# Kernel tuning notes

Hardware: AMD Instinct MI355X
Metric: run time of the kernel (lower is better)

The kernel has to match this reference:

```python
import jax, jax.numpy as jnp
import numpy as np

H = 8   # hidden size
I = 4   # input size
O = 4   # output size


def setup_inputs() -> dict:
    key = jax.random.key(0)
    ks = jax.random.split(key, 7)
    B, T = 4096, 2048
    s_ih = 1.0 / np.sqrt(H)
    x = jax.random.normal(ks[0], (B, T, I), dtype=jnp.float32)
    W_ih = jax.random.uniform(ks[1], (3 * H, I), minval=-s_ih, maxval=s_ih, dtype=jnp.float32)
    W_hh = jax.random.uniform(ks[2], (3 * H, H), minval=-s_ih, maxval=s_ih, dtype=jnp.float32)
    b_ih = jax.random.uniform(ks[3], (3 * H,), minval=-s_ih, maxval=s_ih, dtype=jnp.float32)
    b_hh = jax.random.uniform(ks[4], (3 * H,), minval=-s_ih, maxval=s_ih, dtype=jnp.float32)
    W_fc = jax.random.uniform(ks[5], (O, H), minval=-s_ih, maxval=s_ih, dtype=jnp.float32)
    b_fc = jax.random.uniform(ks[6], (O,), minval=-s_ih, maxval=s_ih, dtype=jnp.float32)
    return {"x": x, "W_ih": W_ih, "W_hh": W_hh, "b_ih": b_ih, "b_hh": b_hh,
            "W_fc": W_fc, "b_fc": b_fc}


def _gru(x, W_ih, W_hh, b_ih, b_hh):
    # x: [B, T, I] (batch_first). Precompute input-gate projections once.
    xg = jnp.einsum('bti,gi->btg', x, W_ih) + b_ih          # [B, T, 3H]
    B = x.shape[0]
    h0 = jnp.zeros((B, H), dtype=x.dtype)

    def step(h, xg_t):
        gh = h @ W_hh.T + b_hh                               # [B, 3H]
        xr, xz, xn = xg_t[:, :H], xg_t[:, H:2 * H], xg_t[:, 2 * H:]
        hr, hz, hn = gh[:, :H], gh[:, H:2 * H], gh[:, 2 * H:]
        r = jax.nn.sigmoid(xr + hr)
        z = jax.nn.sigmoid(xz + hz)
        n = jnp.tanh(xn + r * hn)
        h_new = (1.0 - z) * n + z * h
        return h_new, h_new

    _, hs = jax.lax.scan(step, h0, jnp.swapaxes(xg, 0, 1))  # hs: [T, B, H]
    return jnp.swapaxes(hs, 0, 1)                            # [B, T, H]


def reference(x, W_ih, W_hh, b_ih, b_hh, W_fc, b_fc):
    gru_out = _gru(x, W_ih, W_hh, b_ih, b_hh)                # [B, T, H]
    return jnp.einsum('bth,oh->bto', gru_out, W_fc) + b_fc   # [B, T, O]
```

## Files before the change

### kernel.cpp

```cpp
#include <hip/hip_runtime.h>


#define GRU_T 2048
#define GRU_H 8
#define GRU_I 4
#define GRU_O 4
#define PFD   8

#define DPP_ROR(n) (0x120 + (n))

template <int CTRL>
__device__ __forceinline__ float dpp_movf(float v) {
    return __int_as_float(
        __builtin_amdgcn_mov_dpp(__float_as_int(v), CTRL, 0xf, 0xf, true));
}

__device__ __forceinline__ float fast_rcp(float x)  { return __builtin_amdgcn_rcpf(x); }
__device__ __forceinline__ float fast_exp2(float x) { return __builtin_amdgcn_exp2f(x); }

__global__ __launch_bounds__(64, 1) void gru_fc_kernel(
    const float* __restrict__ x,
    const float* __restrict__ W_ih,
    const float* __restrict__ W_hh,
    const float* __restrict__ b_ih,
    const float* __restrict__ b_hh,
    const float* __restrict__ W_fc,
    const float* __restrict__ b_fc,
    float* __restrict__ out)
{
    const int tid = blockIdx.x * 64 + (int)threadIdx.x;
    const int b   = tid >> 4;
    const int q   = tid & 15;
    const int g   = (q >> 3) & 1;
    const int m   = q & 7;
    const int o   = q & 3;
    const bool hi = (q & 8) != 0;

    const float SR = -1.4426950408889634f;
    const float SZ =  1.4426950408889634f;
    const float SN =  2.8853900817779268f;

    const float SG   = g ? SZ : SR;
    const int   gate = g ? 1 : 0;

    float whA[8], whn[8], wf[8];
#pragma unroll
    for (int r = 0; r < 8; ++r) {
        const int k = (m - r) & 7;
        whA[r] = SG * W_hh[(gate * GRU_H + m) * GRU_H + k];
        whn[r] = SN * W_hh[(2 * GRU_H + m) * GRU_H + k];
        wf[r]  = W_fc[o * GRU_H + k];
    }
    float wiA[4], win[4];
#pragma unroll
    for (int k = 0; k < 4; ++k) {
        wiA[k] = SG * W_ih[(gate * GRU_H + m) * GRU_I + k];
        win[k] = SN * W_ih[(2 * GRU_H + m) * GRU_I + k];
    }
    const float bA  = SG * (b_ih[gate * GRU_H + m] + b_hh[gate * GRU_H + m]);
    const float bxn = SN * b_ih[2 * GRU_H + m];
    const float bhn = SN * b_hh[2 * GRU_H + m];
    const float bo  = b_fc[o];

    float hprev = 0.0f;
    float bank0 = 0.0f, bank1 = 0.0f, bank2 = 0.0f;

    const float4* __restrict__ xp = reinterpret_cast<const float4*>(x) + (size_t)b * GRU_T;
    float* __restrict__ op = out + (size_t)b * GRU_T * GRU_O + q;

    float4 bufA[PFD], bufB[PFD];
#pragma unroll
    for (int j = 0; j < PFD; ++j) bufA[j] = xp[j];

#define GRU_STEP(XC, TCUR, JM)                                                 \
    do {                                                                       \
        const float4 xc = (XC);                                                \
               \
        const float xA  = fmaf(wiA[1], xc.y, fmaf(wiA[0], xc.x, bA));          \
        const float xB  = fmaf(wiA[3], xc.w, wiA[2] * xc.z);                   \
        const float xn_ = fmaf(win[3], xc.w, fmaf(win[2], xc.z,                \
                          fmaf(win[1], xc.y, fmaf(win[0], xc.x, bxn))));       \
        const float onemh = 1.0f - hprev;                                      \
                            \
        const float r1 = dpp_movf<DPP_ROR(1)>(hprev);                          \
        const float r2 = dpp_movf<DPP_ROR(2)>(hprev);                          \
        const float r3 = dpp_movf<DPP_ROR(3)>(hprev);                          \
        const float r4 = dpp_movf<DPP_ROR(4)>(hprev);                          \
        const float r5 = dpp_movf<DPP_ROR(5)>(hprev);                          \
        const float r6 = dpp_movf<DPP_ROR(6)>(hprev);                          \
        const float r7 = dpp_movf<DPP_ROR(7)>(hprev);                          \
                        \
        const float tA = fmaf(whA[1], r1, fmaf(whA[0], hprev, xA));            \
        const float tB = fmaf(whA[3], r3, fmaf(whA[2], r2, xB));               \
        const float tC = fmaf(whA[5], r5, whA[4] * r4);                        \
        const float tD = fmaf(whA[7], r7, whA[6] * r6);                        \
        const float aOwn = (tA + tB) + (tC + tD);                              \
                           \
        const float sOwn = fast_rcp(1.0f + fast_exp2(aOwn));                   \
                        \
        const float sSib = dpp_movf<DPP_ROR(8)>(sOwn);                         \
        const float rg   = hi ? sSib : sOwn;                                   \
        const float omz  = hi ? sOwn : sSib;                                   \
                         \
        const float nA = fmaf(whn[3], r3, fmaf(whn[2], r2,                     \
                         fmaf(whn[1], r1, fmaf(whn[0], hprev, bhn))));         \
        const float nB = fmaf(whn[7], r7, fmaf(whn[6], r6,                     \
                         fmaf(whn[5], r5, whn[4] * r4)));                      \
        const float ahn = nA + nB;                                             \
                         \
        const float fA = fmaf(wf[3], r3, fmaf(wf[2], r2,                       \
                         fmaf(wf[1], r1, fmaf(wf[0], hprev, bo))));            \
        const float fB = fmaf(wf[7], r7, fmaf(wf[6], r6,                       \
                         fmaf(wf[5], r5, wf[4] * r4)));                        \
        const float fc = fA + fB;                                              \
                                              \
        const float c1  = fmaf(omz, onemh, hprev);                             \
        const float m2z = -2.0f * omz;                                         \
        const float yn  = fmaf(rg, ahn, xn_);                                  \
        const float u   = fast_rcp(1.0f + fast_exp2(yn));                      \
        hprev = fmaf(m2z, u, c1);                 \
                   \
        if (((JM) & 3) == 1)      bank0 = fc;                                  \
        else if (((JM) & 3) == 2) bank1 = fc;                                  \
        else if (((JM) & 3) == 3) bank2 = fc;                                  \
        else if ((TCUR) != 0) {                                                \
            const float v01 = (q & 4) ? bank1 : bank0;                         \
            const float v23 = (q & 4) ? fc    : bank2;                         \
            const float val = (q & 8) ? v23   : v01;                           \
            op[(size_t)((TCUR) - 4) * GRU_O] = val;                            \
        }                                                                      \
    } while (0)

    for (int tb = 0; tb < GRU_T; tb += 2 * PFD) {
#pragma unroll
        for (int j = 0; j < PFD; ++j) bufB[j] = xp[tb + PFD + j];
#pragma unroll
        for (int j = 0; j < PFD; ++j) GRU_STEP(bufA[j], tb + j, j);
        const int tn = (tb + 2 * PFD) & (GRU_T - 1);
#pragma unroll
        for (int j = 0; j < PFD; ++j) bufA[j] = xp[tn + j];
#pragma unroll
        for (int j = 0; j < PFD; ++j) GRU_STEP(bufB[j], tb + PFD + j, j);
    }

    {
        const float r1 = dpp_movf<DPP_ROR(1)>(hprev);
        const float r2 = dpp_movf<DPP_ROR(2)>(hprev);
        const float r3 = dpp_movf<DPP_ROR(3)>(hprev);
        const float r4 = dpp_movf<DPP_ROR(4)>(hprev);
        const float r5 = dpp_movf<DPP_ROR(5)>(hprev);
        const float r6 = dpp_movf<DPP_ROR(6)>(hprev);
        const float r7 = dpp_movf<DPP_ROR(7)>(hprev);
        const float fA = fmaf(wf[3], r3, fmaf(wf[2], r2,
                         fmaf(wf[1], r1, fmaf(wf[0], hprev, bo))));
        const float fB = fmaf(wf[7], r7, fmaf(wf[6], r6,
                         fmaf(wf[5], r5, wf[4] * r4)));
        const float fc = fA + fB;
        const float v01 = (q & 4) ? bank1 : bank0;
        const float v23 = (q & 4) ? fc    : bank2;
        const float val = (q & 8) ? v23   : v01;
        op[(size_t)(GRU_T - 4) * GRU_O] = val;
    }
#undef GRU_STEP
}

extern "C" void kernel_launch(void* const* d_in, const int* in_sizes, int n_in,
                              void* d_out, int out_size, void* d_ws, size_t ws_size,
                              hipStream_t stream) {
    const float* x    = (const float*)d_in[0];
    const float* W_ih = (const float*)d_in[1];
    const float* W_hh = (const float*)d_in[2];
    const float* b_ih = (const float*)d_in[3];
    const float* b_hh = (const float*)d_in[4];
    const float* W_fc = (const float*)d_in[5];
    const float* b_fc = (const float*)d_in[6];
    float* out = (float*)d_out;

    const int B = in_sizes[0] / (GRU_T * GRU_I);
    dim3 grid((unsigned)(B * 16 / 64)), block(64);
    hipLaunchKernelGGL(gru_fc_kernel, grid, block, 0, stream,
                       x, W_ih, W_hh, b_ih, b_hh, W_fc, b_fc, out);
}
```

Before: 422.9 us.

## Interleave two batch recurrences per thread and halve the grid

Each 16-lane group now runs the GRU recurrence for two batch elements, interleaving their steps so the two independent dependency chains can hide each other's DPP and transcendental latency. The grid shrinks by half and the prefetch depth drops from 8 to 4 per stream to keep register use in check. The cost is that fewer wavefronts are launched, so some SIMDs may sit idle. Each wave also does twice the serial work.

```diff
diff --git a/kernel.cpp b/kernel.cpp
--- a/kernel.cpp
+++ b/kernel.cpp
@@ -5,7 +5,7 @@
 #define GRU_H 8
 #define GRU_I 4
 #define GRU_O 4
-#define PFD   8
+#define PFD   4
 
 #define DPP_ROR(n) (0x120 + (n))
 
@@ -29,12 +29,15 @@
     float* __restrict__ out)
 {
     const int tid = blockIdx.x * 64 + (int)threadIdx.x;
-    const int b   = tid >> 4;
+    const int G   = tid >> 4;
     const int q   = tid & 15;
     const int g   = (q >> 3) & 1;
     const int m   = q & 7;
     const int o   = q & 3;
     const bool hi = (q & 8) != 0;
+
+    const int eA = 2 * G;
+    const int eB = 2 * G + 1;
 
     const float SR = -1.4426950408889634f;
     const float SZ =  1.4426950408889634f;
@@ -62,106 +65,123 @@
     const float bhn = SN * b_hh[2 * GRU_H + m];
     const float bo  = b_fc[o];
 
-    float hprev = 0.0f;
-    float bank0 = 0.0f, bank1 = 0.0f, bank2 = 0.0f;
-
-    const float4* __restrict__ xp = reinterpret_cast<const float4*>(x) + (size_t)b * GRU_T;
-    float* __restrict__ op = out + (size_t)b * GRU_T * GRU_O + q;
-
-    float4 bufA[PFD], bufB[PFD];
-#pragma unroll
-    for (int j = 0; j < PFD; ++j) bufA[j] = xp[j];
-
-#define GRU_STEP(XC, TCUR, JM)                                                 \
+    float hprevA = 0.0f, bank0A = 0.0f, bank1A = 0.0f, bank2A = 0.0f;
+    float hprevB = 0.0f, bank0B = 0.0f, bank1B = 0.0f, bank2B = 0.0f;
+
+    const float4* __restrict__ xpA = reinterpret_cast<const float4*>(x) + (size_t)eA * GRU_T;
+    const float4* __restrict__ xpB = reinterpret_cast<const float4*>(x) + (size_t)eB * GRU_T;
+    float* __restrict__ opA = out + (size_t)eA * GRU_T * GRU_O + q;
+    float* __restrict__ opB = out + (size_t)eB * GRU_T * GRU_O + q;
+
+    float4 pingA[PFD], pongA[PFD], pingB[PFD], pongB[PFD];
+#pragma unroll
+    for (int j = 0; j < PFD; ++j) { pingA[j] = xpA[j]; pingB[j] = xpB[j]; }
+
+#define GRU_STEP(S, XC, TCUR, JM)                                              \
     do {                                                                       \
         const float4 xc = (XC);                                                \
-               \
-        const float xA  = fmaf(wiA[1], xc.y, fmaf(wiA[0], xc.x, bA));          \
-        const float xB  = fmaf(wiA[3], xc.w, wiA[2] * xc.z);                   \
-        const float xn_ = fmaf(win[3], xc.w, fmaf(win[2], xc.z,                \
-                          fmaf(win[1], xc.y, fmaf(win[0], xc.x, bxn))));       \
-        const float onemh = 1.0f - hprev;                                      \
+        const float xA_  = fmaf(wiA[1], xc.y, fmaf(wiA[0], xc.x, bA));         \
+        const float xB_  = fmaf(wiA[3], xc.w, wiA[2] * xc.z);                  \
+        const float xn_  = fmaf(win[3], xc.w, fmaf(win[2], xc.z,               \
+                           fmaf(win[1], xc.y, fmaf(win[0], xc.x, bxn))));      \
+        const float onemh = 1.0f - hprev##S;                                   \
                             \
-        const float r1 = dpp_movf<DPP_ROR(1)>(hprev);                          \
-        const float r2 = dpp_movf<DPP_ROR(2)>(hprev);                          \
-        const float r3 = dpp_movf<DPP_ROR(3)>(hprev);                          \
-        const float r4 = dpp_movf<DPP_ROR(4)>(hprev);                          \
-        const float r5 = dpp_movf<DPP_ROR(5)>(hprev);                          \
-        const float r6 = dpp_movf<DPP_ROR(6)>(hprev);                          \
-        const float r7 = dpp_movf<DPP_ROR(7)>(hprev);                          \
+        const float r1 = dpp_movf<DPP_ROR(1)>(hprev##S);                       \
+        const float r2 = dpp_movf<DPP_ROR(2)>(hprev##S);                       \
+        const float r3 = dpp_movf<DPP_ROR(3)>(hprev##S);                       \
+        const float r4 = dpp_movf<DPP_ROR(4)>(hprev##S);                       \
+        const float r5 = dpp_movf<DPP_ROR(5)>(hprev##S);                       \
+        const float r6 = dpp_movf<DPP_ROR(6)>(hprev##S);                       \
+        const float r7 = dpp_movf<DPP_ROR(7)>(hprev##S);                       \
                         \
-        const float tA = fmaf(whA[1], r1, fmaf(whA[0], hprev, xA));            \
-        const float tB = fmaf(whA[3], r3, fmaf(whA[2], r2, xB));               \
+        const float tA = fmaf(whA[1], r1, fmaf(whA[0], hprev##S, xA_));        \
+        const float tB = fmaf(whA[3], r3, fmaf(whA[2], r2, xB_));              \
         const float tC = fmaf(whA[5], r5, whA[4] * r4);                        \
         const float tD = fmaf(whA[7], r7, whA[6] * r6);                        \
         const float aOwn = (tA + tB) + (tC + tD);                              \
-                           \
+            \
         const float sOwn = fast_rcp(1.0f + fast_exp2(aOwn));                   \
-                        \
         const float sSib = dpp_movf<DPP_ROR(8)>(sOwn);                         \
         const float rg   = hi ? sSib : sOwn;                                   \
         const float omz  = hi ? sOwn : sSib;                                   \
-                         \
+                                                             \
         const float nA = fmaf(whn[3], r3, fmaf(whn[2], r2,                     \
-                         fmaf(whn[1], r1, fmaf(whn[0], hprev, bhn))));         \
+                         fmaf(whn[1], r1, fmaf(whn[0], hprev##S, bhn))));      \
         const float nB = fmaf(whn[7], r7, fmaf(whn[6], r6,                     \
                          fmaf(whn[5], r5, whn[4] * r4)));                      \
         const float ahn = nA + nB;                                             \
                          \
         const float fA = fmaf(wf[3], r3, fmaf(wf[2], r2,                       \
-                         fmaf(wf[1], r1, fmaf(wf[0], hprev, bo))));            \
+                         fmaf(wf[1], r1, fmaf(wf[0], hprev##S, bo))));         \
         const float fB = fmaf(wf[7], r7, fmaf(wf[6], r6,                       \
                          fmaf(wf[5], r5, wf[4] * r4)));                        \
-        const float fc = fA + fB;                                              \
-                                              \
-        const float c1  = fmaf(omz, onemh, hprev);                             \
+        const float fcv = fA + fB;                                             \
+                                                                     \
+        const float c1  = fmaf(omz, onemh, hprev##S);                          \
         const float m2z = -2.0f * omz;                                         \
         const float yn  = fmaf(rg, ahn, xn_);                                  \
         const float u   = fast_rcp(1.0f + fast_exp2(yn));                      \
-        hprev = fmaf(m2z, u, c1);                 \
-                   \
-        if (((JM) & 3) == 1)      bank0 = fc;                                  \
-        else if (((JM) & 3) == 2) bank1 = fc;                                  \
-        else if (((JM) & 3) == 3) bank2 = fc;                                  \
+        hprev##S = fmaf(m2z, u, c1);              \
+                         \
+        if ((JM) == 1)      bank0##S = fcv;                                    \
+        else if ((JM) == 2) bank1##S = fcv;                                    \
+        else if ((JM) == 3) bank2##S = fcv;                                    \
         else if ((TCUR) != 0) {                                                \
-            const float v01 = (q & 4) ? bank1 : bank0;                         \
-            const float v23 = (q & 4) ? fc    : bank2;                         \
-            const float val = (q & 8) ? v23   : v01;                           \
-            op[(size_t)((TCUR) - 4) * GRU_O] = val;                            \
+            const float v01 = (q & 4) ? bank1##S : bank0##S;                   \
+            const float v23 = (q & 4) ? fcv      : bank2##S;                   \
+            const float val = (q & 8) ? v23      : v01;                        \
+            op##S[(size_t)((TCUR) - 4) * GRU_O] = val;                         \
         }                                                                      \
     } while (0)
 
     for (int tb = 0; tb < GRU_T; tb += 2 * PFD) {
 #pragma unroll
-        for (int j = 0; j < PFD; ++j) bufB[j] = xp[tb + PFD + j];
-#pragma unroll
-        for (int j = 0; j < PFD; ++j) GRU_STEP(bufA[j], tb + j, j);
+        for (int j = 0; j < PFD; ++j) {
+            pongA[j] = xpA[tb + PFD + j];
+            pongB[j] = xpB[tb + PFD + j];
+        }
+#pragma unroll
+        for (int j = 0; j < PFD; ++j) {
+            GRU_STEP(A, pingA[j], tb + j, j);
+            GRU_STEP(B, pingB[j], tb + j, j);
+        }
         const int tn = (tb + 2 * PFD) & (GRU_T - 1);
 #pragma unroll
-        for (int j = 0; j < PFD; ++j) bufA[j] = xp[tn + j];
-#pragma unroll
-        for (int j = 0; j < PFD; ++j) GRU_STEP(bufB[j], tb + PFD + j, j);
+        for (int j = 0; j < PFD; ++j) {
+            pingA[j] = xpA[tn + j];
+            pingB[j] = xpB[tn + j];
+        }
+#pragma unroll
+        for (int j = 0; j < PFD; ++j) {
+            GRU_STEP(A, pongA[j], tb + PFD + j, j);
+            GRU_STEP(B, pongB[j], tb + PFD + j, j);
+        }
     }
 
-    {
-        const float r1 = dpp_movf<DPP_ROR(1)>(hprev);
-        const float r2 = dpp_movf<DPP_ROR(2)>(hprev);
-        const float r3 = dpp_movf<DPP_ROR(3)>(hprev);
-        const float r4 = dpp_movf<DPP_ROR(4)>(hprev);
-        const float r5 = dpp_movf<DPP_ROR(5)>(hprev);
-        const float r6 = dpp_movf<DPP_ROR(6)>(hprev);
-        const float r7 = dpp_movf<DPP_ROR(7)>(hprev);
-        const float fA = fmaf(wf[3], r3, fmaf(wf[2], r2,
-                         fmaf(wf[1], r1, fmaf(wf[0], hprev, bo))));
-        const float fB = fmaf(wf[7], r7, fmaf(wf[6], r6,
-                         fmaf(wf[5], r5, wf[4] * r4)));
-        const float fc = fA + fB;
-        const float v01 = (q & 4) ? bank1 : bank0;
-        const float v23 = (q & 4) ? fc    : bank2;
-        const float val = (q & 8) ? v23   : v01;
-        op[(size_t)(GRU_T - 4) * GRU_O] = val;
-    }
+#define GRU_EPI(S)                                                             \
+    do {                                                                       \
+        const float r1 = dpp_movf<DPP_ROR(1)>(hprev##S);                       \
+        const float r2 = dpp_movf<DPP_ROR(2)>(hprev##S);                       \
+        const float r3 = dpp_movf<DPP_ROR(3)>(hprev##S);                       \
+        const float r4 = dpp_movf<DPP_ROR(4)>(hprev##S);                       \
+        const float r5 = dpp_movf<DPP_ROR(5)>(hprev##S);                       \
+        const float r6 = dpp_movf<DPP_ROR(6)>(hprev##S);                       \
+        const float r7 = dpp_movf<DPP_ROR(7)>(hprev##S);                       \
+        const float fA = fmaf(wf[3], r3, fmaf(wf[2], r2,                       \
+                         fmaf(wf[1], r1, fmaf(wf[0], hprev##S, bo))));         \
+        const float fB = fmaf(wf[7], r7, fmaf(wf[6], r6,                       \
+                         fmaf(wf[5], r5, wf[4] * r4)));                        \
+        const float fcv = fA + fB;                                             \
+        const float v01 = (q & 4) ? bank1##S : bank0##S;                       \
+        const float v23 = (q & 4) ? fcv      : bank2##S;                       \
+        const float val = (q & 8) ? v23      : v01;                            \
+        op##S[(size_t)(GRU_T - 4) * GRU_O] = val;                              \
+    } while (0)
+
+    GRU_EPI(A);
+    GRU_EPI(B);
 #undef GRU_STEP
+#undef GRU_EPI
 }
 
 extern "C" void kernel_launch(void* const* d_in, const int* in_sizes, int n_in,
@@ -177,7 +197,7 @@
     float* out = (float*)d_out;
 
     const int B = in_sizes[0] / (GRU_T * GRU_I);
-    dim3 grid((unsigned)(B * 16 / 64)), block(64);
+    dim3 grid((unsigned)(B * 16 / (64 * 2))), block(64);
     hipLaunchKernelGGL(gru_fc_kernel, grid, block, 0, stream,
                        x, W_ih, W_hh, b_ih, b_hh, W_fc, b_fc, out);
 }
```

After: 727.2 us. 1.72x slower.
